# Optimization experiments

Measured on AMD Instinct MI355X. Metric: run time of the kernel, lower is better.

Reference implementation:

```python
import jax, jax.numpy as jnp
import numpy as np

B, D, K = 8192, 2048, 2048  # batch, input dim, output_dim (must be equal: k==d required by call())


def setup_inputs() -> dict:
    key = jax.random.key(0)
    k1, k2, k3, k4 = jax.random.split(key, 4)
    lim_w = float(np.sqrt(6.0 / (K + D)))        # glorot_uniform for W (k,d)
    lim_v = float(np.sqrt(6.0 / (2 * D + K)))    # glorot_uniform for V (2d,k)
    return {
        "e1": jax.random.normal(k1, (B, D), jnp.float32),
        "e2": jax.random.normal(k2, (B, D), jnp.float32),
        "W": jax.random.uniform(k3, (K, D), jnp.float32, -lim_w, lim_w),
        "V": jax.random.uniform(k4, (2 * D, K), jnp.float32, -lim_v, lim_v),
        "b": jnp.zeros((K,), jnp.float32),
    }


def reference(e1, e2, W, V, b):
    # Faithful translation of the active call() of NeuralTensorDiagLayer.
    # call() tiles flatten(e1) k times and reshapes to (B, d, k); index algebra
    # shows x[p, q, r] = e1[(p*d+q)%B, r] * e2[(p*d+q)%B, r] * W[q, r]
    # (requires k == d for the W broadcast), then mean over the last axis (size k).
    # Equivalent efficient form: u = ((e1*e2) @ W.T)/k, then gather rows (p*d+q)%B.
    bsz, d = e1.shape
    k = W.shape[0]
    ff = jnp.concatenate([e1, e2], axis=-1) @ V              # (B, k) feedforward GEMM
    u = ((e1 * e2) @ W.T) / k                                # (B, k) diag bilinear, mean over k
    cols = jnp.arange(k)[None, :]                            # (1, k)
    rows = (jnp.arange(bsz)[:, None] * d + cols) % bsz       # (B, k) batch-mixing index from tile/reshape
    z = u[rows, cols]                                        # (B, k)
    return jnp.tanh(z + ff + b)
```

## Files before the change

### kernel.cpp

```cpp
#include <hip/hip_runtime.h>
#include <hip/hip_bf16.h>

typedef __bf16 bf16;
typedef bf16 bf16x8 __attribute__((ext_vector_type(8)));
typedef bf16 bf16x4 __attribute__((ext_vector_type(4)));
typedef float f32x4 __attribute__((ext_vector_type(4)));

#define AS1 __attribute__((address_space(1)))
#define AS3 __attribute__((address_space(3)))

__device__ __forceinline__ void gload_lds16(const void* g, void* l) {
    __builtin_amdgcn_global_load_lds((const AS1 void*)g, (AS3 void*)l, 16, 0, 0);
}

__device__ __forceinline__ float tanh_fast(float x) {
    float xx = fminf(fmaxf(x, -15.0f), 15.0f);
    float e = __expf(2.0f * xx);
    return (e - 1.0f) / (e + 1.0f);
}

__global__ __launch_bounds__(256) void conv_x_zs(
    const float* __restrict__ e1, const float* __restrict__ e2,
    const float* __restrict__ W, bf16* __restrict__ Xb, float* __restrict__ zs)
{
    const int r = blockIdx.x;
    const int t = threadIdx.x;
    const int c = r & 2047, m = r >> 11;
    const size_t rb = (size_t)r * 2048;

    const float4* p1 = (const float4*)(e1 + rb) + t * 2;
    const float4* p2 = (const float4*)(e2 + rb) + t * 2;
    const float4* pw = (const float4*)(W + (size_t)c * 2048) + t * 2;
    float4 a0 = p1[0], a1 = p1[1];
    float4 b0 = p2[0], b1 = p2[1];
    float4 w0 = pw[0], w1 = pw[1];

    float dot = a0.x*b0.x*w0.x + a0.y*b0.y*w0.y + a0.z*b0.z*w0.z + a0.w*b0.w*w0.w
              + a1.x*b1.x*w1.x + a1.y*b1.y*w1.y + a1.z*b1.z*w1.z + a1.w*b1.w*w1.w;

    bf16x8 xa, xb;
    xa[0]=(bf16)a0.x; xa[1]=(bf16)a0.y; xa[2]=(bf16)a0.z; xa[3]=(bf16)a0.w;
    xa[4]=(bf16)a1.x; xa[5]=(bf16)a1.y; xa[6]=(bf16)a1.z; xa[7]=(bf16)a1.w;
    xb[0]=(bf16)b0.x; xb[1]=(bf16)b0.y; xb[2]=(bf16)b0.z; xb[3]=(bf16)b0.w;
    xb[4]=(bf16)b1.x; xb[5]=(bf16)b1.y; xb[6]=(bf16)b1.z; xb[7]=(bf16)b1.w;

    *(bf16x8*)(Xb + (size_t)r * 4096 + t * 8)        = xa;
    *(bf16x8*)(Xb + (size_t)r * 4096 + 2048 + t * 8) = xb;

    #pragma unroll
    for (int off = 32; off; off >>= 1) dot += __shfl_xor(dot, off);
    __shared__ float red[4];
    if ((t & 63) == 0) red[t >> 6] = dot;
    __syncthreads();
    if (t == 0) zs[m * 2048 + c] = (red[0] + red[1] + red[2] + red[3]) * (1.0f / 2048.0f);
}

__global__ __launch_bounds__(256) void conv_vt(const float* __restrict__ V,
                                               bf16* __restrict__ Vt)
{
    __shared__ float tile[64][65];
    const int k0 = (blockIdx.x >> 5) * 64;
    const int c0 = (blockIdx.x & 31) * 64;
    const int t = threadIdx.x;
    const int rr = t >> 4;
    const int cc = (t & 15) * 4;

    #pragma unroll
    for (int r4 = 0; r4 < 4; ++r4) {
        int row = r4 * 16 + rr;
        float4 v = *(const float4*)(V + (size_t)(k0 + row) * 2048 + c0 + cc);
        tile[row][cc + 0] = v.x; tile[row][cc + 1] = v.y;
        tile[row][cc + 2] = v.z; tile[row][cc + 3] = v.w;
    }
    __syncthreads();
    #pragma unroll
    for (int r4 = 0; r4 < 4; ++r4) {
        int crow = r4 * 16 + rr;
        bf16x4 o;
        o[0] = (bf16)tile[cc + 0][crow];
        o[1] = (bf16)tile[cc + 1][crow];
        o[2] = (bf16)tile[cc + 2][crow];
        o[3] = (bf16)tile[cc + 3][crow];
        *(bf16x4*)(Vt + (size_t)(c0 + crow) * 4096 + k0 + cc) = o;
    }
}

__global__ __launch_bounds__(256, 2) void gemm_ep(
    const bf16* __restrict__ Xb, const bf16* __restrict__ Vt,
    const float* __restrict__ zs, const float* __restrict__ bias,
    float* __restrict__ out)
{
    extern __shared__ char smem[];
    const int tid  = threadIdx.x;
    const int lane = tid & 63;
    const int wid  = tid >> 6;
    const int wr = wid >> 1, wc = wid & 1;
    const int mtile = blockIdx.x >> 4;
    const int ntile = blockIdx.x & 15;
    const int row0 = mtile * 256, col0 = ntile * 128;

    const int lr   = lane & 15;
    const int lkb  = (lane >> 4) * 16;
    const int keyx = ((lr >> 1) & 3) << 4;

    const int srow  = tid >> 2;
    const int scb   = ((tid & 3) * 16) ^ (((srow >> 1) & 3) << 4);
    const bf16* Asrc = Xb + (size_t)(row0 + srow) * 4096 + (scb >> 1);
    const bf16* Bsrc = Vt + (size_t)(col0 + srow) * 4096 + (scb >> 1);

    f32x4 acc[8][4] = {};
    bf16x8 aA[8], bB[4];

    auto stage = [&](int b, int kt) {
        char* Al = smem + b * 24576 + tid * 16;
        char* Bl = smem + b * 24576 + 16384 + tid * 16;
        const bf16* Ag = Asrc + kt * 32;
        const bf16* Bg = Bsrc + kt * 32;
        #pragma unroll
        for (int r = 0; r < 4; ++r)
            gload_lds16(Ag + (size_t)(r * 64) * 4096, Al + r * 4096);
        #pragma unroll
        for (int r = 0; r < 2; ++r)
            gload_lds16(Bg + (size_t)(r * 64) * 4096, Bl + r * 4096);
    };
    auto rdAB = [&](int b) {
        const char* Ab = smem + b * 24576;
        const char* Bb = Ab + 16384;
        #pragma unroll
        for (int i = 0; i < 8; ++i) {
            const int R = wr * 128 + i * 16 + lr;
            aA[i] = *(const bf16x8*)(Ab + R * 64 + (lkb ^ keyx));
        }
        #pragma unroll
        for (int j = 0; j < 4; ++j) {
            const int R = wc * 64 + j * 16 + lr;
            bB[j] = *(const bf16x8*)(Bb + R * 64 + (lkb ^ keyx));
        }
    };
    auto mm = [&]() {
        __builtin_amdgcn_s_setprio(1);
        #pragma unroll
        for (int i = 0; i < 8; ++i)
            #pragma unroll
            for (int j = 0; j < 4; ++j)
                acc[i][j] = __builtin_amdgcn_mfma_f32_16x16x32_bf16(
                    aA[i], bB[j], acc[i][j], 0, 0, 0);
        __builtin_amdgcn_s_setprio(0);
    };

    stage(0, 0);
    stage(1, 1);
    asm volatile("s_waitcnt vmcnt(6)" ::: "memory");
    __builtin_amdgcn_s_barrier();

    #pragma unroll 3
    for (int t = 0; t < 126; ++t) {
        const int rb = t % 3;
        const int sb = (t + 2) % 3;
        stage(sb, t + 2);
        rdAB(rb);
        mm();
        asm volatile("s_waitcnt vmcnt(6)" ::: "memory");
        __builtin_amdgcn_s_barrier();
    }
    rdAB(0);
    mm();
    asm volatile("s_waitcnt vmcnt(0)" ::: "memory");
    __builtin_amdgcn_s_barrier();
    rdAB(1);
    mm();

    const int lq = lane >> 4;
    #pragma unroll
    for (int j = 0; j < 4; ++j) {
        const int ccol = col0 + wc * 64 + j * 16 + lr;
        const float bb = bias[ccol];
        float zrow[4];
        #pragma unroll
        for (int q = 0; q < 4; ++q) zrow[q] = zs[q * 2048 + ccol] + bb;
        #pragma unroll
        for (int i = 0; i < 8; ++i) {
            const int prow = row0 + wr * 128 + i * 16 + lq * 4;
            #pragma unroll
            for (int q = 0; q < 4; ++q)
                out[(size_t)(prow + q) * 2048 + ccol] =
                    tanh_fast(acc[i][j][q] + zrow[q]);
        }
    }
}

extern "C" void kernel_launch(void* const* d_in, const int* in_sizes, int n_in,
                              void* d_out, int out_size, void* d_ws, size_t ws_size,
                              hipStream_t stream) {
    const float* e1 = (const float*)d_in[0];
    const float* e2 = (const float*)d_in[1];
    const float* W  = (const float*)d_in[2];
    const float* V  = (const float*)d_in[3];
    const float* b  = (const float*)d_in[4];
    float* out = (float*)d_out;

    char* ws = (char*)d_ws;
    bf16*  Xb = (bf16*)ws;
    bf16*  Vt = (bf16*)(ws + (size_t)64 * 1024 * 1024);
    float* zs = (float*)(ws + (size_t)80 * 1024 * 1024);

    conv_x_zs<<<8192, 256, 0, stream>>>(e1, e2, W, Xb, zs);
    conv_vt<<<2048, 256, 0, stream>>>(V, Vt);

    hipFuncSetAttribute((const void*)gemm_ep,
                        hipFuncAttributeMaxDynamicSharedMemorySize, 73728);
    gemm_ep<<<512, 256, 73728, stream>>>(Xb, Vt, zs, b, out);
}
```

Before: 196.5 us.

## Shrink GEMM tile to 128x128 and load B straight from global into registers

The GEMM block tile drops from 256x128 to 128x128, which doubles the grid to 1024 blocks. Only A is now staged in LDS through the triple-buffered async pipeline, while each wave reads its B fragments directly from global memory into registers every k-step. LDS use falls to 24 KB and the launch bound rises to 3 blocks per SM, aiming for higher occupancy and less LDS traffic. In exchange, B loads are not prefetched, so their global/L2 latency sits on the critical path each iteration, and B data is no longer shared through LDS, which raises L2 traffic.

```diff
diff --git a/kernel.cpp b/kernel.cpp
--- a/kernel.cpp
+++ b/kernel.cpp
@@ -85,7 +85,7 @@
     }
 }
 
-__global__ __launch_bounds__(256, 2) void gemm_ep(
+__global__ __launch_bounds__(256, 3) void gemm_ep(
     const bf16* __restrict__ Xb, const bf16* __restrict__ Vt,
     const float* __restrict__ zs, const float* __restrict__ bias,
     float* __restrict__ out)
@@ -97,7 +97,7 @@
     const int wr = wid >> 1, wc = wid & 1;
     const int mtile = blockIdx.x >> 4;
     const int ntile = blockIdx.x & 15;
-    const int row0 = mtile * 256, col0 = ntile * 128;
+    const int row0 = mtile * 128, col0 = ntile * 128;
 
     const int lr   = lane & 15;
     const int lkb  = (lane >> 4) * 16;
@@ -106,41 +106,35 @@
     const int srow  = tid >> 2;
     const int scb   = ((tid & 3) * 16) ^ (((srow >> 1) & 3) << 4);
     const bf16* Asrc = Xb + (size_t)(row0 + srow) * 4096 + (scb >> 1);
-    const bf16* Bsrc = Vt + (size_t)(col0 + srow) * 4096 + (scb >> 1);
-
-    f32x4 acc[8][4] = {};
-    bf16x8 aA[8], bB[4];
+
+    const bf16* Bln = Vt + (size_t)(col0 + wc * 64 + lr) * 4096 + (lkb >> 1);
+
+    f32x4 acc[4][4] = {};
+    bf16x8 aA[4], bB[4];
 
     auto stage = [&](int b, int kt) {
-        char* Al = smem + b * 24576 + tid * 16;
-        char* Bl = smem + b * 24576 + 16384 + tid * 16;
+        char* Al = smem + b * 8192 + tid * 16;
         const bf16* Ag = Asrc + kt * 32;
-        const bf16* Bg = Bsrc + kt * 32;
-        #pragma unroll
-        for (int r = 0; r < 4; ++r)
-            gload_lds16(Ag + (size_t)(r * 64) * 4096, Al + r * 4096);
-        #pragma unroll
-        for (int r = 0; r < 2; ++r)
-            gload_lds16(Bg + (size_t)(r * 64) * 4096, Bl + r * 4096);
-    };
-    auto rdAB = [&](int b) {
-        const char* Ab = smem + b * 24576;
-        const char* Bb = Ab + 16384;
-        #pragma unroll
-        for (int i = 0; i < 8; ++i) {
-            const int R = wr * 128 + i * 16 + lr;
+        gload_lds16(Ag, Al);
+        gload_lds16(Ag + (size_t)64 * 4096, Al + 4096);
+    };
+    auto ldB = [&](int kt) {
+        #pragma unroll
+        for (int j = 0; j < 4; ++j)
+            bB[j] = *(const bf16x8*)(Bln + (size_t)j * 16 * 4096 + kt * 32);
+    };
+    auto rdA = [&](int b) {
+        const char* Ab = smem + b * 8192;
+        #pragma unroll
+        for (int i = 0; i < 4; ++i) {
+            const int R = wr * 64 + i * 16 + lr;
             aA[i] = *(const bf16x8*)(Ab + R * 64 + (lkb ^ keyx));
         }
-        #pragma unroll
-        for (int j = 0; j < 4; ++j) {
-            const int R = wc * 64 + j * 16 + lr;
-            bB[j] = *(const bf16x8*)(Bb + R * 64 + (lkb ^ keyx));
-        }
     };
     auto mm = [&]() {
         __builtin_amdgcn_s_setprio(1);
         #pragma unroll
-        for (int i = 0; i < 8; ++i)
+        for (int i = 0; i < 4; ++i)
             #pragma unroll
             for (int j = 0; j < 4; ++j)
                 acc[i][j] = __builtin_amdgcn_mfma_f32_16x16x32_bf16(
@@ -150,24 +144,27 @@
 
     stage(0, 0);
     stage(1, 1);
-    asm volatile("s_waitcnt vmcnt(6)" ::: "memory");
+    asm volatile("s_waitcnt vmcnt(2)" ::: "memory");
     __builtin_amdgcn_s_barrier();
 
     #pragma unroll 3
     for (int t = 0; t < 126; ++t) {
         const int rb = t % 3;
         const int sb = (t + 2) % 3;
+        ldB(t);
         stage(sb, t + 2);
-        rdAB(rb);
+        rdA(rb);
         mm();
-        asm volatile("s_waitcnt vmcnt(6)" ::: "memory");
+        asm volatile("s_waitcnt vmcnt(2)" ::: "memory");
         __builtin_amdgcn_s_barrier();
     }
-    rdAB(0);
+    ldB(126);
+    rdA(0);
     mm();
     asm volatile("s_waitcnt vmcnt(0)" ::: "memory");
     __builtin_amdgcn_s_barrier();
-    rdAB(1);
+    ldB(127);
+    rdA(1);
     mm();
 
     const int lq = lane >> 4;
@@ -179,8 +176,8 @@
         #pragma unroll
         for (int q = 0; q < 4; ++q) zrow[q] = zs[q * 2048 + ccol] + bb;
         #pragma unroll
-        for (int i = 0; i < 8; ++i) {
-            const int prow = row0 + wr * 128 + i * 16 + lq * 4;
+        for (int i = 0; i < 4; ++i) {
+            const int prow = row0 + wr * 64 + i * 16 + lq * 4;
             #pragma unroll
             for (int q = 0; q < 4; ++q)
                 out[(size_t)(prow + q) * 2048 + ccol] =
@@ -208,6 +205,6 @@
     conv_vt<<<2048, 256, 0, stream>>>(V, Vt);
 
     hipFuncSetAttribute((const void*)gemm_ep,
-                        hipFuncAttributeMaxDynamicSharedMemorySize, 73728);
-    gemm_ep<<<512, 256, 73728, stream>>>(Xb, Vt, zs, b, out);
-}
+                        hipFuncAttributeMaxDynamicSharedMemorySize, 24576);
+    gemm_ep<<<1024, 256, 24576, stream>>>(Xb, Vt, zs, b, out);
+}
```

Result: slower. 340.9 us (+73.5%).
